# Optimization experiments

Hardware: AMD Instinct MI355X
Metric: run time of the kernel (lower is better)

The kernel has to match this reference:

```python
import jax, jax.numpy as jnp
import numpy as np

TEMPERATURE = 0.07
BASE_TEMPERATURE = 0.07


def _pairwise_euclid(x):
    # torch.cdist(x, x, p=2), with safe sqrt (zero grad at zero distance)
    sq = jnp.sum(x * x, axis=1)
    d2 = sq[:, None] + sq[None, :] - 2.0 * (x @ x.T)
    d2 = jnp.maximum(d2, 0.0)
    safe = jnp.where(d2 > 0.0, d2, 1.0)
    return jnp.where(d2 > 0.0, jnp.sqrt(safe), 0.0)


def setup_inputs() -> dict:
    key = jax.random.key(0)
    k1, k2 = jax.random.split(key)
    features = jax.random.normal(k1, (1024, 2, 512), dtype=jnp.float32)
    labels = jax.random.uniform(k2, (1024,), dtype=jnp.float32)
    return {"features": features, "labels": labels}


def reference(features, labels):
    B, V, D = features.shape
    N = B * V
    # torch.cat(torch.unbind(features, dim=1), dim=0): views stacked -> [N, D]
    cf = features.transpose(1, 0, 2).reshape(N, D)
    lab = jnp.tile(labels, V)  # label of row i is labels[i % B]

    dist = _pairwise_euclid(cf)              # [N, N]
    logits = -dist / TEMPERATURE
    eye = jnp.eye(N, dtype=logits.dtype)
    w = jnp.exp(logits) * (1.0 - eye)        # exp(logits) with l == i excluded

    dis = jnp.abs(lab[:, None] - lab[None, :])  # |y_i - y_j|, symmetric

    # negative[i, j] = sum_{l != i, |y_l - y_i| >= |y_i - y_j|} exp(logits[i, l])
    # computed per-row via sort + suffix cumsum + searchsorted (O(N^2 log N))
    order = jnp.argsort(dis, axis=1)
    sorted_d = jnp.take_along_axis(dis, order, axis=1)
    sorted_w = jnp.take_along_axis(w, order, axis=1)
    suffix = jnp.flip(jnp.cumsum(jnp.flip(sorted_w, axis=1), axis=1), axis=1)
    suffix = jnp.concatenate([suffix, jnp.zeros((N, 1), suffix.dtype)], axis=1)  # [N, N+1]
    # side='left': counts entries strictly < d, so suffix[idx] sums all >= d (ties incl.)
    idx = jax.vmap(lambda sd, d: jnp.searchsorted(sd, d, side='left'))(sorted_d, dis)
    negative = jnp.take_along_axis(suffix, idx, axis=1)
    negative = negative * (1.0 - eye) + eye  # diag set to 1 (log -> 0)

    logits_z = logits * (1.0 - eye)          # logits[i, i] = 0
    log_prob = logits_z - jnp.log(negative)
    mean_log_prob_pos = jnp.sum(log_prob, axis=1) / (N - 1)
    loss = -(TEMPERATURE / BASE_TEMPERATURE) * jnp.mean(mean_log_prob_pos)
    return loss
```

## Files before the change

kernel.cpp:

```cpp
#include <hip/hip_runtime.h>
#include <math.h>


#define NN 2048
#define BB 1024
#define DD 512
#define NT 256
#define NEGINF (-INFINITY)
#define CS 64.0f

typedef short s16x8 __attribute__((ext_vector_type(8)));
typedef float f32x4 __attribute__((ext_vector_type(4)));

__device__ __forceinline__ const float* cf_row(const float* F, int i) {
    return F + ((size_t)(i & (BB - 1)) * 2 + (size_t)(i >> 10)) * DD;
}

__device__ __forceinline__ unsigned bf_rne(float x) {
    const unsigned u = __float_as_uint(x);
    return (u + 0x7FFFu + ((u >> 16) & 1u)) >> 16;
}
__device__ __forceinline__ float bf_val(unsigned h) {
    return __uint_as_float(h << 16);
}

__global__ __launch_bounds__(512) void prep_sort_kernel(const float* __restrict__ F,
                                                        const float* __restrict__ labels,
                                                        ushort* __restrict__ Ahi,
                                                        ushort* __restrict__ Alo,
                                                        float* __restrict__ sq,
                                                        float* __restrict__ slab,
                                                        int* __restrict__ sj) {
    __shared__ float lab[BB];
    const int blk = blockIdx.x;
    const int t = threadIdx.x;

    if (blk < 256) {
        const int lane = t & 63;
        const int w = t >> 6;
        const int i = blk * 8 + w;
        const float* src = cf_row(F, i);
        const float4 v0 = reinterpret_cast<const float4*>(src)[lane];
        const float4 v1 = reinterpret_cast<const float4*>(src)[lane + 64];
        float ss = v0.x * v0.x + v0.y * v0.y + v0.z * v0.z + v0.w * v0.w
                 + v1.x * v1.x + v1.y * v1.y + v1.z * v1.z + v1.w * v1.w;
        #pragma unroll
        for (int st = 32; st > 0; st >>= 1) ss += __shfl_down(ss, st);
        if (lane == 0) sq[i] = ss;

        const float a[8] = {v0.x, v0.y, v0.z, v0.w, v1.x, v1.y, v1.z, v1.w};
        ushort h[8], l[8];
        #pragma unroll
        for (int e = 0; e < 8; ++e) {
            const unsigned hb = bf_rne(a[e]);
            h[e] = (ushort)hb;
            l[e] = (ushort)bf_rne(a[e] - bf_val(hb));
        }
        const size_t base = (size_t)i * DD;
        *reinterpret_cast<ushort4*>(&Ahi[base + lane * 4])       = make_ushort4(h[0], h[1], h[2], h[3]);
        *reinterpret_cast<ushort4*>(&Ahi[base + 256 + lane * 4]) = make_ushort4(h[4], h[5], h[6], h[7]);
        *reinterpret_cast<ushort4*>(&Alo[base + lane * 4])       = make_ushort4(l[0], l[1], l[2], l[3]);
        *reinterpret_cast<ushort4*>(&Alo[base + 256 + lane * 4]) = make_ushort4(l[4], l[5], l[6], l[7]);
    } else {
        lab[t] = labels[t];
        lab[t + 512] = labels[t + 512];
        __syncthreads();
        const int e = (blk - 256) * 512 + t;
        const float li = lab[e];
        int rank = 0;
        const float4* l4 = reinterpret_cast<const float4*>(lab);
        #pragma unroll 4
        for (int j = 0; j < BB / 4; ++j) {
            const float4 v = l4[j];
            const int j0 = j * 4;
            rank += (v.x < li) || (v.x == li && (j0 + 0) < e);
            rank += (v.y < li) || (v.y == li && (j0 + 1) < e);
            rank += (v.z < li) || (v.z == li && (j0 + 2) < e);
            rank += (v.w < li) || (v.w == li && (j0 + 3) < e);
        }
        slab[2 * rank]     = li;
        slab[2 * rank + 1] = li;
        sj[2 * rank]     = e;
        sj[2 * rank + 1] = e + BB;
    }
}

#define TM 128
#define TN 64
#define TK 32
__global__ __launch_bounds__(256) void gemm_dist_kernel(const ushort* __restrict__ Ahi,
                                                        const ushort* __restrict__ Alo,
                                                        const float* __restrict__ sq,
                                                        const int* __restrict__ sj,
                                                        float* __restrict__ distp) {
    __shared__ ushort Ah[4][TM][8];
    __shared__ ushort Al[4][TM][8];
    __shared__ ushort Bh[4][TN][8];
    __shared__ ushort Bl[4][TN][8];
    __shared__ int   sjcA[TM];
    __shared__ int   sjcB[TN];
    __shared__ float sqA[TM];
    __shared__ float sqB[TN];

    const int t = threadIdx.x;
    const int lane = t & 63;
    const int w = t >> 6;

    const int id = blockIdx.x;
    int by = (int)((__fsqrt_rn(4.0f * (float)id + 1.0f) - 1.0f) * 0.5f);
    while ((by + 1) * (by + 2) <= id) ++by;
    while (by * (by + 1) > id) --by;
    const int bx = id - by * (by + 1);
    const int row0 = by * TM;
    const int col0 = bx * TN;
    const bool below = (bx < 2 * by);

    if (t < TM) {
        const int s = sj[row0 + t];
        sjcA[t] = s; sqA[t] = sq[s];
    } else if (t < TM + TN) {
        const int u = t - TM;
        const int s = sj[col0 + u];
        sjcB[u] = s; sqB[u] = sq[s];
    }
    __syncthreads();
    const int rr = t >> 2;
    const int cq = t & 3;
    const size_t gA0 = (size_t)sjcA[rr] * DD + cq * 8;
    const size_t gA1 = (size_t)sjcA[64 + rr] * DD + cq * 8;
    const size_t gB0 = (size_t)sjcB[rr] * DD + cq * 8;

    f32x4 acc[2][4] = {};
    const int m = lane & 15;
    const int q = lane >> 4;

    for (int kt = 0; kt < DD / TK; ++kt) {
        __syncthreads();
        const size_t ko = (size_t)kt * TK;
        *reinterpret_cast<int4*>(&Ah[cq][rr][0])      = *reinterpret_cast<const int4*>(&Ahi[gA0 + ko]);
        *reinterpret_cast<int4*>(&Al[cq][rr][0])      = *reinterpret_cast<const int4*>(&Alo[gA0 + ko]);
        *reinterpret_cast<int4*>(&Ah[cq][64 + rr][0]) = *reinterpret_cast<const int4*>(&Ahi[gA1 + ko]);
        *reinterpret_cast<int4*>(&Al[cq][64 + rr][0]) = *reinterpret_cast<const int4*>(&Alo[gA1 + ko]);
        *reinterpret_cast<int4*>(&Bh[cq][rr][0])      = *reinterpret_cast<const int4*>(&Ahi[gB0 + ko]);
        *reinterpret_cast<int4*>(&Bl[cq][rr][0])      = *reinterpret_cast<const int4*>(&Alo[gB0 + ko]);
        __syncthreads();

        s16x8 fah[2], fal[2], fbh[4], fbl[4];
        #pragma unroll
        for (int mt = 0; mt < 2; ++mt) {
            fah[mt] = *reinterpret_cast<const s16x8*>(&Ah[q][w * 32 + mt * 16 + m][0]);
            fal[mt] = *reinterpret_cast<const s16x8*>(&Al[q][w * 32 + mt * 16 + m][0]);
        }
        #pragma unroll
        for (int nt = 0; nt < 4; ++nt) {
            fbh[nt] = *reinterpret_cast<const s16x8*>(&Bh[q][nt * 16 + m][0]);
            fbl[nt] = *reinterpret_cast<const s16x8*>(&Bl[q][nt * 16 + m][0]);
        }
        #pragma unroll
        for (int mt = 0; mt < 2; ++mt)
            #pragma unroll
            for (int nt = 0; nt < 4; ++nt) {
                acc[mt][nt] = __builtin_amdgcn_mfma_f32_16x16x32_bf16(fah[mt], fbh[nt], acc[mt][nt], 0, 0, 0);
                acc[mt][nt] = __builtin_amdgcn_mfma_f32_16x16x32_bf16(fah[mt], fbl[nt], acc[mt][nt], 0, 0, 0);
                acc[mt][nt] = __builtin_amdgcn_mfma_f32_16x16x32_bf16(fal[mt], fbh[nt], acc[mt][nt], 0, 0, 0);
            }
    }

    #pragma unroll
    for (int mt = 0; mt < 2; ++mt) {
        const int lr0 = w * 32 + mt * 16 + q * 4;
        #pragma unroll
        for (int nt = 0; nt < 4; ++nt) {
            const int lc = nt * 16 + m;
            float o[4];
            #pragma unroll
            for (int r = 0; r < 4; ++r) {
                const float d2 = sqA[lr0 + r] + sqB[lc] - 2.0f * acc[mt][nt][r];
                o[r] = (d2 > 0.f) ? sqrtf(d2) : 0.f;
            }
            #pragma unroll
            for (int r = 0; r < 4; ++r)
                distp[(size_t)(row0 + lr0 + r) * NN + col0 + lc] = o[r];
            if (below) {
                const float4 o4 = make_float4(o[0], o[1], o[2], o[3]);
                *reinterpret_cast<float4*>(&distp[(size_t)(col0 + lc) * NN + row0 + lr0]) = o4;
            }
        }
    }
}

__device__ __forceinline__ int bs_right(const float* key, float d, int lo, int hi) {
    while (lo < hi) {
        const int mid = (lo + hi) >> 1;
        if (key[mid] >= d) hi = mid; else lo = mid + 1;
    }
    return lo;
}
__device__ __forceinline__ int bs_left(const float* key, float d, int lo, int hi) {
    while (lo < hi) {
        const int mid = (lo + hi) >> 1;
        if (key[mid] < d) hi = mid; else lo = mid + 1;
    }
    return lo;
}

__global__ __launch_bounds__(256) void row_kernel(const float* __restrict__ distp,
                                                  const float* __restrict__ slab,
                                                  double* __restrict__ rowval) {
    __shared__ float key[NN];
    __shared__ float Pf[NN];
    __shared__ float Sf[NN + 1];
    __shared__ float wmxA[4], wmxB[4], wps[4], wss[4];
    __shared__ double wDA[4], wLA[4], wDB[4], wLB[4];

    const int pr = blockIdx.x;
    const int rA = 2 * pr, rB = 2 * pr + 1;
    const int t = threadIdx.x;
    const int lane = t & 63;
    const int w = t >> 6;
    const float x = slab[rA];
    const float negInvT = -1.0f / 0.07f;
    const float* drowA = &distp[(size_t)rA * NN];
    const float* drowB = &distp[(size_t)rB * NN];

    #pragma unroll
    for (int e = 0; e < 2; ++e) {
        const int p4 = t + e * NT;
        const float4 l4 = reinterpret_cast<const float4*>(slab)[p4];
        key[p4 * 4 + 0] = fabsf(l4.x - x);
        key[p4 * 4 + 1] = fabsf(l4.y - x);
        key[p4 * 4 + 2] = fabsf(l4.z - x);
        key[p4 * 4 + 3] = fabsf(l4.w - x);
    }
    const int cb = t * 8;
    float vA[8], vB[8];
    double dsumA = 0.0, dsumB = 0.0;
    float mxA = NEGINF, mxB = NEGINF;
    #pragma unroll
    for (int e = 0; e < 2; ++e) {
        const float4 a4 = reinterpret_cast<const float4*>(drowA)[2 * t + e];
        const float4 b4 = reinterpret_cast<const float4*>(drowB)[2 * t + e];
        const float av[4] = {a4.x, a4.y, a4.z, a4.w};
        const float bv[4] = {b4.x, b4.y, b4.z, b4.w};
        #pragma unroll
        for (int c = 0; c < 4; ++c) {
            const int pc = cb + e * 4 + c;
            if (pc == rA) vA[e * 4 + c] = NEGINF;
            else { const float vv = av[c] * negInvT; vA[e * 4 + c] = vv; mxA = fmaxf(mxA, vv); dsumA += (double)av[c]; }
            if (pc == rB) vB[e * 4 + c] = NEGINF;
            else { const float vv = bv[c] * negInvT; vB[e * 4 + c] = vv; mxB = fmaxf(mxB, vv); dsumB += (double)bv[c]; }
        }
    }
    #pragma unroll
    for (int st = 32; st > 0; st >>= 1) {
        mxA = fmaxf(mxA, __shfl_down(mxA, st));
        mxB = fmaxf(mxB, __shfl_down(mxB, st));
    }
    if (lane == 0) { wmxA[w] = mxA; wmxB[w] = mxB; }
    __syncthreads();
    const float MA = fmaxf(fmaxf(wmxA[0], wmxA[1]), fmaxf(wmxA[2], wmxA[3]));
    const float MB = fmaxf(fmaxf(wmxB[0], wmxB[1]), fmaxf(wmxB[2], wmxB[3]));

    int L8[8], R8[8];
    const int a = cb, b = cb + 7;
    {
        const int le = (rA - 1 < b) ? rA - 1 : b;
        if (a <= le) {
            const float da = key[a];
            const int Ra = bs_right(key, da, rA, NN);
            int Rl = Ra;
            if (le > a) Rl = bs_right(key, key[le], rA, Ra);
            for (int p = a; p <= le; ++p) {
                const float d = key[p];
                int R;
                if (p == a) R = Ra;
                else if (p == le) R = Rl;
                else R = bs_right(key, d, Rl, Ra);
                int L = p + 1;
                while (L < rA && key[L] == d) ++L;
                L8[p - a] = L; R8[p - a] = R;
            }
        }
        const int rs = (rA + 1 > a) ? rA + 1 : a;
        if (rs <= b) {
            const float dr = key[rs];
            const int Lr = bs_left(key, dr, 0, rA);
            int Lb = Lr;
            if (b > rs) Lb = bs_left(key, key[b], 0, Lr);
            for (int p = rs; p <= b; ++p) {
                const float d = key[p];
                int L;
                if (p == rs) L = Lr;
                else if (p == b) L = Lb;
                else L = bs_left(key, d, Lb, Lr);
                int R = p;
                while (R > rA && key[R - 1] == d) --R;
                L8[p - a] = L; R8[p - a] = R;
            }
        }
        if (rA >= a && rA <= b) { L8[rA - a] = rA; R8[rA - a] = rA; }
    }

    double lnsumA = 0.0;
    {
        float e8[8];
        #pragma unroll
        for (int jj = 0; jj < 8; ++jj) e8[jj] = __expf(vA[jj] - MA + CS);
        float ex[8], sx[8], xofsP, xofsS;
        {
            float run = 0.f;
            #pragma unroll
            for (int jj = 0; jj < 8; ++jj) { ex[jj] = run; run += e8[jj]; }
            float incP = run;
            #pragma unroll
            for (int st = 1; st < 64; st <<= 1) {
                const float nm = __shfl_up(incP, st);
                if (lane >= st) incP += nm;
            }
            xofsP = __shfl_up(incP, 1);
            if (lane == 0) xofsP = 0.f;
            if (lane == 63) wps[w] = incP;

            float runS = 0.f;
            #pragma unroll
            for (int jj = 7; jj >= 0; --jj) { runS += e8[jj]; sx[jj] = runS; }
            float incS = runS;
            #pragma unroll
            for (int st = 1; st < 64; st <<= 1) {
                const float nm = __shfl_down(incS, st);
                if (lane + st < 64) incS += nm;
            }
            xofsS = __shfl_down(incS, 1);
            if (lane == 63) xofsS = 0.f;
            if (lane == 0) wss[w] = incS;
        }
        __syncthreads();
        #pragma unroll
        for (int ww = 0; ww < 3; ++ww)
            if (ww < w) xofsP += wps[ww];
        #pragma unroll
        for (int ww = 1; ww < 4; ++ww)
            if (ww > w) xofsS += wss[ww];
        #pragma unroll
        for (int jj = 0; jj < 8; ++jj) Pf[cb + jj] = ex[jj] + xofsP;
        #pragma unroll
        for (int jj = 0; jj < 8; ++jj) Sf[cb + jj] = sx[jj] + xofsS;
        if (t == 0) Sf[NN] = 0.f;
        __syncthreads();
        const float MBA = MA - CS;
        #pragma unroll
        for (int jj = 0; jj < 8; ++jj) {
            const int p = cb + jj;
            if (p == rA) continue;
            const float s = fmaxf(Pf[L8[jj]] + Sf[R8[jj]], 1e-38f);
            lnsumA += (double)(MBA + __logf(s));
        }
    }
    __syncthreads();

    double lnsumB = 0.0;
    {
        float e8[8];
        #pragma unroll
        for (int jj = 0; jj < 8; ++jj) e8[jj] = __expf(vB[jj] - MB + CS);
        float ex[8], sx[8], xofsP, xofsS;
        {
            float run = 0.f;
            #pragma unroll
            for (int jj = 0; jj < 8; ++jj) { ex[jj] = run; run += e8[jj]; }
            float incP = run;
            #pragma unroll
            for (int st = 1; st < 64; st <<= 1) {
                const float nm = __shfl_up(incP, st);
                if (lane >= st) incP += nm;
            }
            xofsP = __shfl_up(incP, 1);
            if (lane == 0) xofsP = 0.f;
            if (lane == 63) wps[w] = incP;

            float runS = 0.f;
            #pragma unroll
            for (int jj = 7; jj >= 0; --jj) { runS += e8[jj]; sx[jj] = runS; }
            float incS = runS;
            #pragma unroll
            for (int st = 1; st < 64; st <<= 1) {
                const float nm = __shfl_down(incS, st);
                if (lane + st < 64) incS += nm;
            }
            xofsS = __shfl_down(incS, 1);
            if (lane == 63) xofsS = 0.f;
            if (lane == 0) wss[w] = incS;
        }
        __syncthreads();
        #pragma unroll
        for (int ww = 0; ww < 3; ++ww)
            if (ww < w) xofsP += wps[ww];
        #pragma unroll
        for (int ww = 1; ww < 4; ++ww)
            if (ww > w) xofsS += wss[ww];
        #pragma unroll
        for (int jj = 0; jj < 8; ++jj) Pf[cb + jj] = ex[jj] + xofsP;
        #pragma unroll
        for (int jj = 0; jj < 8; ++jj) Sf[cb + jj] = sx[jj] + xofsS;
        if (t == 0) Sf[NN] = 0.f;
        __syncthreads();
        const float MBB = MB - CS;
        #pragma unroll
        for (int jj = 0; jj < 8; ++jj) {
            const int p = cb + jj;
            if (p == rB) continue;
            const float s = fmaxf(Pf[L8[jj]] + Sf[R8[jj]], 1e-38f);
            lnsumB += (double)(MBB + __logf(s));
        }
    }

    #pragma unroll
    for (int st = 32; st > 0; st >>= 1) {
        dsumA  += __shfl_down(dsumA, st);
        lnsumA += __shfl_down(lnsumA, st);
        dsumB  += __shfl_down(dsumB, st);
        lnsumB += __shfl_down(lnsumB, st);
    }
    if (lane == 0) { wDA[w] = dsumA; wLA[w] = lnsumA; wDB[w] = dsumB; wLB[w] = lnsumB; }
    __syncthreads();
    if (t == 0) {
        rowval[rA] = (-(wDA[0] + wDA[1] + wDA[2] + wDA[3]) / 0.07)
                   - (wLA[0] + wLA[1] + wLA[2] + wLA[3]);
        rowval[rB] = (-(wDB[0] + wDB[1] + wDB[2] + wDB[3]) / 0.07)
                   - (wLB[0] + wLB[1] + wLB[2] + wLB[3]);
    }
}

__global__ __launch_bounds__(256) void finalize_kernel(const double* __restrict__ rowval,
                                                       float* __restrict__ out) {
    __shared__ double red[NT];
    const int t = threadIdx.x;
    double s = 0.0;
    for (int j = t; j < NN; j += NT) s += rowval[j];
    red[t] = s;
    __syncthreads();
    for (int ofs = NT / 2; ofs > 0; ofs >>= 1) {
        if (t < ofs) red[t] += red[t + ofs];
        __syncthreads();
    }
    if (t == 0) {
        out[0] = (float)(-red[0] / ((double)NN * (double)(NN - 1)));
    }
}

extern "C" void kernel_launch(void* const* d_in, const int* in_sizes, int n_in,
                              void* d_out, int out_size, void* d_ws, size_t ws_size,
                              hipStream_t stream) {
    const float* features = (const float*)d_in[0];
    const float* labels   = (const float*)d_in[1];
    float* out = (float*)d_out;

    char* ws = (char*)d_ws;
    size_t off = 0;
    float*  sq     = (float*) (ws + off); off += NN * sizeof(float);
    float*  slab   = (float*) (ws + off); off += NN * sizeof(float);
    int*    sj     = (int*)   (ws + off); off += NN * sizeof(int);
    double* rowval = (double*)(ws + off); off += NN * sizeof(double);
    ushort* Ahi    = (ushort*)(ws + off); off += (size_t)NN * DD * sizeof(ushort);
    ushort* Alo    = (ushort*)(ws + off); off += (size_t)NN * DD * sizeof(ushort);
    float*  distp  = (float*) (ws + off); off += (size_t)NN * NN * sizeof(float);

    prep_sort_kernel<<<258, 512, 0, stream>>>(features, labels, Ahi, Alo, sq, slab, sj);
    gemm_dist_kernel<<<16 * 17, NT, 0, stream>>>(Ahi, Alo, sq, sj, distp);
    row_kernel<<<NN / 2, NT, 0, stream>>>(distp, slab, rowval);
    finalize_kernel<<<1, NT, 0, stream>>>(rowval, out);
}
```

Baseline: 143.4 us.

## Fuse dual-row scans, drop shared key array, search labels from global memory

Removes the shared-memory key array and runs the binary searches directly on the global label array, recomputing |y - x| on the fly. The max-reduction barrier now comes after the search, so the global latency can overlap. The two per-row prefix/suffix scans are merged into one pass with separate shared buffers, cutting the number of block-wide barriers. In exchange, the binary searches now issue dependent global/L2 loads instead of LDS reads.

```diff
diff --git a/kernel.cpp b/kernel.cpp
--- a/kernel.cpp
+++ b/kernel.cpp
@@ -189,17 +189,19 @@
     }
 }
 
-__device__ __forceinline__ int bs_right(const float* key, float d, int lo, int hi) {
+__device__ __forceinline__ int bs_right_g(const float* __restrict__ slab, float x,
+                                          float d, int lo, int hi) {
     while (lo < hi) {
         const int mid = (lo + hi) >> 1;
-        if (key[mid] >= d) hi = mid; else lo = mid + 1;
+        if (fabsf(slab[mid] - x) >= d) hi = mid; else lo = mid + 1;
     }
     return lo;
 }
-__device__ __forceinline__ int bs_left(const float* key, float d, int lo, int hi) {
+__device__ __forceinline__ int bs_left_g(const float* __restrict__ slab, float x,
+                                         float d, int lo, int hi) {
     while (lo < hi) {
         const int mid = (lo + hi) >> 1;
-        if (key[mid] < d) hi = mid; else lo = mid + 1;
+        if (fabsf(slab[mid] - x) < d) hi = mid; else lo = mid + 1;
     }
     return lo;
 }
@@ -207,10 +209,11 @@
 __global__ __launch_bounds__(256) void row_kernel(const float* __restrict__ distp,
                                                   const float* __restrict__ slab,
                                                   double* __restrict__ rowval) {
-    __shared__ float key[NN];
-    __shared__ float Pf[NN];
-    __shared__ float Sf[NN + 1];
-    __shared__ float wmxA[4], wmxB[4], wps[4], wss[4];
+    __shared__ float PfA[NN];
+    __shared__ float SfA[NN];
+    __shared__ float PfB[NN];
+    __shared__ float SfB[NN];
+    __shared__ float wmxA[4], wmxB[4], wpsA[4], wssA[4], wpsB[4], wssB[4];
     __shared__ double wDA[4], wLA[4], wDB[4], wLB[4];
 
     const int pr = blockIdx.x;
@@ -222,17 +225,8 @@
     const float negInvT = -1.0f / 0.07f;
     const float* drowA = &distp[(size_t)rA * NN];
     const float* drowB = &distp[(size_t)rB * NN];
-
-    #pragma unroll
-    for (int e = 0; e < 2; ++e) {
-        const int p4 = t + e * NT;
-        const float4 l4 = reinterpret_cast<const float4*>(slab)[p4];
-        key[p4 * 4 + 0] = fabsf(l4.x - x);
-        key[p4 * 4 + 1] = fabsf(l4.y - x);
-        key[p4 * 4 + 2] = fabsf(l4.z - x);
-        key[p4 * 4 + 3] = fabsf(l4.w - x);
-    }
     const int cb = t * 8;
+
     float vA[8], vB[8];
     double dsumA = 0.0, dsumB = 0.0;
     float mxA = NEGINF, mxB = NEGINF;
@@ -257,159 +251,129 @@
         mxB = fmaxf(mxB, __shfl_down(mxB, st));
     }
     if (lane == 0) { wmxA[w] = mxA; wmxB[w] = mxB; }
-    __syncthreads();
-    const float MA = fmaxf(fmaxf(wmxA[0], wmxA[1]), fmaxf(wmxA[2], wmxA[3]));
-    const float MB = fmaxf(fmaxf(wmxB[0], wmxB[1]), fmaxf(wmxB[2], wmxB[3]));
 
     int L8[8], R8[8];
+    float d8[8];
+    {
+        const float4 s0 = reinterpret_cast<const float4*>(slab)[2 * t];
+        const float4 s1 = reinterpret_cast<const float4*>(slab)[2 * t + 1];
+        d8[0] = fabsf(s0.x - x); d8[1] = fabsf(s0.y - x);
+        d8[2] = fabsf(s0.z - x); d8[3] = fabsf(s0.w - x);
+        d8[4] = fabsf(s1.x - x); d8[5] = fabsf(s1.y - x);
+        d8[6] = fabsf(s1.z - x); d8[7] = fabsf(s1.w - x);
+    }
     const int a = cb, b = cb + 7;
     {
         const int le = (rA - 1 < b) ? rA - 1 : b;
         if (a <= le) {
-            const float da = key[a];
-            const int Ra = bs_right(key, da, rA, NN);
+            const float da = d8[0];
+            const int Ra = bs_right_g(slab, x, da, rA, NN);
             int Rl = Ra;
-            if (le > a) Rl = bs_right(key, key[le], rA, Ra);
+            if (le > a) Rl = bs_right_g(slab, x, d8[le - a], rA, Ra);
             for (int p = a; p <= le; ++p) {
-                const float d = key[p];
+                const float d = d8[p - a];
                 int R;
                 if (p == a) R = Ra;
                 else if (p == le) R = Rl;
-                else R = bs_right(key, d, Rl, Ra);
+                else R = bs_right_g(slab, x, d, Rl, Ra);
                 int L = p + 1;
-                while (L < rA && key[L] == d) ++L;
+                while (L < rA && fabsf(slab[L] - x) == d) ++L;
                 L8[p - a] = L; R8[p - a] = R;
             }
         }
         const int rs = (rA + 1 > a) ? rA + 1 : a;
         if (rs <= b) {
-            const float dr = key[rs];
-            const int Lr = bs_left(key, dr, 0, rA);
+            const float dr = d8[rs - a];
+            const int Lr = bs_left_g(slab, x, dr, 0, rA);
             int Lb = Lr;
-            if (b > rs) Lb = bs_left(key, key[b], 0, Lr);
+            if (b > rs) Lb = bs_left_g(slab, x, d8[b - a], 0, Lr);
             for (int p = rs; p <= b; ++p) {
-                const float d = key[p];
+                const float d = d8[p - a];
                 int L;
                 if (p == rs) L = Lr;
                 else if (p == b) L = Lb;
-                else L = bs_left(key, d, Lb, Lr);
+                else L = bs_left_g(slab, x, d, Lb, Lr);
                 int R = p;
-                while (R > rA && key[R - 1] == d) --R;
+                while (R > rA && fabsf(slab[R - 1] - x) == d) --R;
                 L8[p - a] = L; R8[p - a] = R;
             }
         }
         if (rA >= a && rA <= b) { L8[rA - a] = rA; R8[rA - a] = rA; }
     }
 
-    double lnsumA = 0.0;
+    __syncthreads();
+    const float MA = fmaxf(fmaxf(wmxA[0], wmxA[1]), fmaxf(wmxA[2], wmxA[3]));
+    const float MB = fmaxf(fmaxf(wmxB[0], wmxB[1]), fmaxf(wmxB[2], wmxB[3]));
+
+    float exA[8], sxA[8], exB[8], sxB[8];
+    float xofsPA, xofsSA, xofsPB, xofsSB;
     {
-        float e8[8];
-        #pragma unroll
-        for (int jj = 0; jj < 8; ++jj) e8[jj] = __expf(vA[jj] - MA + CS);
-        float ex[8], sx[8], xofsP, xofsS;
-        {
-            float run = 0.f;
-            #pragma unroll
-            for (int jj = 0; jj < 8; ++jj) { ex[jj] = run; run += e8[jj]; }
-            float incP = run;
-            #pragma unroll
-            for (int st = 1; st < 64; st <<= 1) {
-                const float nm = __shfl_up(incP, st);
-                if (lane >= st) incP += nm;
-            }
-            xofsP = __shfl_up(incP, 1);
-            if (lane == 0) xofsP = 0.f;
-            if (lane == 63) wps[w] = incP;
-
-            float runS = 0.f;
-            #pragma unroll
-            for (int jj = 7; jj >= 0; --jj) { runS += e8[jj]; sx[jj] = runS; }
-            float incS = runS;
-            #pragma unroll
-            for (int st = 1; st < 64; st <<= 1) {
-                const float nm = __shfl_down(incS, st);
-                if (lane + st < 64) incS += nm;
-            }
-            xofsS = __shfl_down(incS, 1);
-            if (lane == 63) xofsS = 0.f;
-            if (lane == 0) wss[w] = incS;
-        }
-        __syncthreads();
-        #pragma unroll
-        for (int ww = 0; ww < 3; ++ww)
-            if (ww < w) xofsP += wps[ww];
-        #pragma unroll
-        for (int ww = 1; ww < 4; ++ww)
-            if (ww > w) xofsS += wss[ww];
-        #pragma unroll
-        for (int jj = 0; jj < 8; ++jj) Pf[cb + jj] = ex[jj] + xofsP;
-        #pragma unroll
-        for (int jj = 0; jj < 8; ++jj) Sf[cb + jj] = sx[jj] + xofsS;
-        if (t == 0) Sf[NN] = 0.f;
-        __syncthreads();
-        const float MBA = MA - CS;
+        float e8A[8], e8B[8];
         #pragma unroll
         for (int jj = 0; jj < 8; ++jj) {
-            const int p = cb + jj;
-            if (p == rA) continue;
-            const float s = fmaxf(Pf[L8[jj]] + Sf[R8[jj]], 1e-38f);
+            e8A[jj] = __expf(vA[jj] - MA + CS);
+            e8B[jj] = __expf(vB[jj] - MB + CS);
+        }
+        float runPA = 0.f, runPB = 0.f;
+        #pragma unroll
+        for (int jj = 0; jj < 8; ++jj) {
+            exA[jj] = runPA; runPA += e8A[jj];
+            exB[jj] = runPB; runPB += e8B[jj];
+        }
+        float runSA = 0.f, runSB = 0.f;
+        #pragma unroll
+        for (int jj = 7; jj >= 0; --jj) {
+            runSA += e8A[jj]; sxA[jj] = runSA;
+            runSB += e8B[jj]; sxB[jj] = runSB;
+        }
+        float incPA = runPA, incPB = runPB, incSA = runSA, incSB = runSB;
+        #pragma unroll
+        for (int st = 1; st < 64; st <<= 1) {
+            const float nPA = __shfl_up(incPA, st);
+            const float nPB = __shfl_up(incPB, st);
+            const float nSA = __shfl_down(incSA, st);
+            const float nSB = __shfl_down(incSB, st);
+            if (lane >= st)      { incPA += nPA; incPB += nPB; }
+            if (lane + st < 64)  { incSA += nSA; incSB += nSB; }
+        }
+        xofsPA = __shfl_up(incPA, 1);
+        xofsPB = __shfl_up(incPB, 1);
+        xofsSA = __shfl_down(incSA, 1);
+        xofsSB = __shfl_down(incSB, 1);
+        if (lane == 0)  { xofsPA = 0.f; xofsPB = 0.f; wssA[w] = incSA; wssB[w] = incSB; }
+        if (lane == 63) { xofsSA = 0.f; xofsSB = 0.f; wpsA[w] = incPA; wpsB[w] = incPB; }
+    }
+    __syncthreads();
+    #pragma unroll
+    for (int ww = 0; ww < 3; ++ww)
+        if (ww < w) { xofsPA += wpsA[ww]; xofsPB += wpsB[ww]; }
+    #pragma unroll
+    for (int ww = 1; ww < 4; ++ww)
+        if (ww > w) { xofsSA += wssA[ww]; xofsSB += wssB[ww]; }
+    #pragma unroll
+    for (int jj = 0; jj < 8; ++jj) {
+        PfA[cb + jj] = exA[jj] + xofsPA;
+        SfA[cb + jj] = sxA[jj] + xofsSA;
+        PfB[cb + jj] = exB[jj] + xofsPB;
+        SfB[cb + jj] = sxB[jj] + xofsSB;
+    }
+    __syncthreads();
+
+    double lnsumA = 0.0, lnsumB = 0.0;
+    const float MBA = MA - CS;
+    const float MBB = MB - CS;
+    #pragma unroll
+    for (int jj = 0; jj < 8; ++jj) {
+        const int p = cb + jj;
+        const int L = L8[jj], R = R8[jj];
+        if (p != rA) {
+            const float sfa = (R < NN) ? SfA[R] : 0.f;
+            const float s = fmaxf(PfA[L] + sfa, 1e-38f);
             lnsumA += (double)(MBA + __logf(s));
         }
-    }
-    __syncthreads();
-
-    double lnsumB = 0.0;
-    {
-        float e8[8];
-        #pragma unroll
-        for (int jj = 0; jj < 8; ++jj) e8[jj] = __expf(vB[jj] - MB + CS);
-        float ex[8], sx[8], xofsP, xofsS;
-        {
-            float run = 0.f;
-            #pragma unroll
-            for (int jj = 0; jj < 8; ++jj) { ex[jj] = run; run += e8[jj]; }
-            float incP = run;
-            #pragma unroll
-            for (int st = 1; st < 64; st <<= 1) {
-                const float nm = __shfl_up(incP, st);
-                if (lane >= st) incP += nm;
-            }
-            xofsP = __shfl_up(incP, 1);
-            if (lane == 0) xofsP = 0.f;
-            if (lane == 63) wps[w] = incP;
-
-            float runS = 0.f;
-            #pragma unroll
-            for (int jj = 7; jj >= 0; --jj) { runS += e8[jj]; sx[jj] = runS; }
-            float incS = runS;
-            #pragma unroll
-            for (int st = 1; st < 64; st <<= 1) {
-                const float nm = __shfl_down(incS, st);
-                if (lane + st < 64) incS += nm;
-            }
-            xofsS = __shfl_down(incS, 1);
-            if (lane == 63) xofsS = 0.f;
-            if (lane == 0) wss[w] = incS;
-        }
-        __syncthreads();
-        #pragma unroll
-        for (int ww = 0; ww < 3; ++ww)
-            if (ww < w) xofsP += wps[ww];
-        #pragma unroll
-        for (int ww = 1; ww < 4; ++ww)
-            if (ww > w) xofsS += wss[ww];
-        #pragma unroll
-        for (int jj = 0; jj < 8; ++jj) Pf[cb + jj] = ex[jj] + xofsP;
-        #pragma unroll
-        for (int jj = 0; jj < 8; ++jj) Sf[cb + jj] = sx[jj] + xofsS;
-        if (t == 0) Sf[NN] = 0.f;
-        __syncthreads();
-        const float MBB = MB - CS;
-        #pragma unroll
-        for (int jj = 0; jj < 8; ++jj) {
-            const int p = cb + jj;
-            if (p == rB) continue;
-            const float s = fmaxf(Pf[L8[jj]] + Sf[R8[jj]], 1e-38f);
+        if (p != rB) {
+            const float sfb = (R < NN) ? SfB[R] : 0.f;
+            const float s = fmaxf(PfB[L] + sfb, 1e-38f);
             lnsumB += (double)(MBB + __logf(s));
         }
     }
```

New measurement: 146.8 us. 1.02x slower.
